# Optimization experiments

Hardware: AMD Instinct MI355X
Metric: run time of the kernel (lower is better)

The kernel has to match this reference:

```python
import jax, jax.numpy as jnp
import numpy as np

N = 32768      # total nodes
B = 64         # graphs
NPG = 512      # nodes per graph
E = 524288     # edges (avg degree 16)
H = 4          # heads
Fh = 64        # per-head dim
C = H * Fh     # 256
FIN = 128
RATIO = 0.5


def gat(x, src, dst, W, a_src, a_dst, bias, n_nodes):
    # PyG GATConv: linear -> add self-loops -> edge softmax over dst -> scatter-add
    h = (x @ W).reshape(n_nodes, H, Fh)
    loop = jnp.arange(n_nodes)
    s = jnp.concatenate([src, loop])
    d = jnp.concatenate([dst, loop])
    es = jnp.sum(h * a_src, axis=-1)  # [N,H]
    ed = jnp.sum(h * a_dst, axis=-1)  # [N,H]
    e = jax.nn.leaky_relu(es[s] + ed[d], 0.2)  # [E+N,H]
    m = jax.ops.segment_max(e, d, num_segments=n_nodes)
    ex = jnp.exp(e - m[d])
    den = jax.ops.segment_sum(ex, d, num_segments=n_nodes)
    alpha = ex / (den[d] + 1e-16)  # [E+N,H]
    out = jax.ops.segment_sum(alpha[:, :, None] * h[s], d, num_segments=n_nodes)
    return out.reshape(n_nodes, C) + bias


def pool(x, sw, sb, tw, tb, n_graphs, n_per):
    # equal-size graphs -> per-graph top-k as a batched top_k
    k = max(1, int(n_per * RATIO))
    scores = jax.nn.sigmoid(x @ sw + sb)[:, 0].reshape(n_graphs, n_per)
    _, idx = jax.lax.top_k(scores, k)  # [B,k]
    xb = x.reshape(n_graphs, n_per, x.shape[-1])
    sel = jnp.take_along_axis(xb, idx[:, :, None], axis=1)
    sel = sel.reshape(n_graphs * k, x.shape[-1])
    return sel @ tw + tb, k


def setup_inputs() -> dict:
    key = jax.random.key(0)
    ks = jax.random.split(key, 24)
    x = jax.random.normal(ks[0], (N, FIN), dtype=jnp.float32)
    # within-graph random edges
    gbase = jnp.repeat(jnp.arange(B, dtype=jnp.int32) * NPG, E // B)
    src = gbase + jax.random.randint(ks[1], (E,), 0, NPG)
    dst = gbase + jax.random.randint(ks[2], (E,), 0, NPG)
    edge_index = jnp.stack([src, dst]).astype(jnp.int32)
    batch = jnp.repeat(jnp.arange(B, dtype=jnp.int32), NPG)
    def lin(k, fi, fo):
        return jax.random.normal(k, (fi, fo), dtype=jnp.float32) / np.sqrt(fi)
    inp = dict(x=x, edge_index=edge_index, batch=batch)
    inp["W1"] = lin(ks[3], FIN, C)
    inp["a_src1"] = jax.random.normal(ks[4], (H, Fh), jnp.float32) / np.sqrt(Fh)
    inp["a_dst1"] = jax.random.normal(ks[5], (H, Fh), jnp.float32) / np.sqrt(Fh)
    inp["b1"] = jnp.zeros((C,), jnp.float32)
    inp["W2"] = lin(ks[6], C, C)
    inp["a_src2"] = jax.random.normal(ks[7], (H, Fh), jnp.float32) / np.sqrt(Fh)
    inp["a_dst2"] = jax.random.normal(ks[8], (H, Fh), jnp.float32) / np.sqrt(Fh)
    inp["b2"] = jnp.zeros((C,), jnp.float32)
    inp["p1_sw"] = lin(ks[9], C, 1)
    inp["p1_sb"] = jnp.zeros((1,), jnp.float32)
    inp["p1_tw"] = lin(ks[10], C, C)
    inp["p1_tb"] = jnp.zeros((C,), jnp.float32)
    inp["p2_sw"] = lin(ks[11], C, 1)
    inp["p2_sb"] = jnp.zeros((1,), jnp.float32)
    inp["p2_tw"] = lin(ks[12], C, C)
    inp["p2_tb"] = jnp.zeros((C,), jnp.float32)
    inp["c1w"] = lin(ks[13], C, 64)
    inp["c1b"] = jnp.zeros((64,), jnp.float32)
    inp["c2w"] = lin(ks[14], 64, 2)
    inp["c2b"] = jnp.zeros((2,), jnp.float32)
    return inp


def reference(x, edge_index, batch, W1, a_src1, a_dst1, b1, W2, a_src2, a_dst2, b2,
              p1_sw, p1_sb, p1_tw, p1_tb, p2_sw, p2_sb, p2_tw, p2_tb,
              c1w, c1b, c2w, c2b):
    src, dst = edge_index[0], edge_index[1]
    h = jax.nn.elu(gat(x, src, dst, W1, a_src1, a_dst1, b1, N))
    h = jax.nn.elu(gat(h, src, dst, W2, a_src2, a_dst2, b2, N))
    # pool1 then pool2 (edge_index after pooling is never consumed by the output path)
    h, k1 = pool(h, p1_sw, p1_sb, p1_tw, p1_tb, B, NPG)
    h, k2 = pool(h, p2_sw, p2_sb, p2_tw, p2_tb, B, k1)
    g = h.reshape(B, k2, C).mean(axis=1)  # global mean pool per graph
    g = jax.nn.relu(g @ c1w + c1b)
    g = g @ c2w + c2b
    return jax.nn.log_softmax(g, axis=1)
```

## Files before the change

kernel.cpp:

```cpp
#include <hip/hip_runtime.h>
#include <hip/hip_bf16.h>
#include <hip/hip_fp16.h>
#include <math.h>

constexpr int NN  = 32768;
constexpr int BG  = 64;
constexpr int NPG = 512;
constexpr int EG  = 524288;
constexpr int EPG = EG / BG;
constexpr int HH  = 4;
constexpr int FH  = 64;
constexpr int CC  = 256;
constexpr int FIN = 128;
constexpr int KP1 = 256;
constexpr int KP2 = 128;
constexpr int NS  = 4;

typedef __attribute__((ext_vector_type(8))) short short8;
typedef __attribute__((ext_vector_type(4))) float f32x4;

__device__ inline float leaky02(float v) { return v > 0.0f ? v : 0.2f * v; }

__device__ inline unsigned short f2bf(float v) {
    __hip_bfloat16 h = __float2bfloat16(v);
    return *(unsigned short*)&h;
}
__device__ inline float bf2f(unsigned short u) {
    __hip_bfloat16 h;
    *(unsigned short*)&h = u;
    return __bfloat162float(h);
}
__device__ inline void split2(float v, unsigned short& hi, unsigned short& lo) {
    hi = f2bf(v);
    lo = f2bf(v - bf2f(hi));
}
__device__ inline void split8(const float* p, short8& hi, short8& lo) {
    const float4 f0 = *(const float4*)p;
    const float4 f1 = *(const float4*)(p + 4);
    unsigned short h, l;
    split2(f0.x, h, l); hi[0] = (short)h; lo[0] = (short)l;
    split2(f0.y, h, l); hi[1] = (short)h; lo[1] = (short)l;
    split2(f0.z, h, l); hi[2] = (short)h; lo[2] = (short)l;
    split2(f0.w, h, l); hi[3] = (short)h; lo[3] = (short)l;
    split2(f1.x, h, l); hi[4] = (short)h; lo[4] = (short)l;
    split2(f1.y, h, l); hi[5] = (short)h; lo[5] = (short)l;
    split2(f1.z, h, l); hi[6] = (short)h; lo[6] = (short)l;
    split2(f1.w, h, l); hi[7] = (short)h; lo[7] = (short)l;
}

__device__ inline unsigned short f2h(float v) {
    __half h = __float2half(v);
    return *(unsigned short*)&h;
}

__device__ inline unsigned int fmap(float v) {
    unsigned int b = __float_as_uint(v);
    return (b & 0x80000000u) ? ~b : (b | 0x80000000u);
}

__device__ inline void acc8h(const unsigned short* p, float a, float* acc) {
    const uint4 u = *(const uint4*)p;
    const __half2* hp = (const __half2*)&u;
    const float2 f0 = __half22float2(hp[0]);
    const float2 f1 = __half22float2(hp[1]);
    const float2 f2 = __half22float2(hp[2]);
    const float2 f3 = __half22float2(hp[3]);
    acc[0] = fmaf(a, f0.x, acc[0]); acc[1] = fmaf(a, f0.y, acc[1]);
    acc[2] = fmaf(a, f1.x, acc[2]); acc[3] = fmaf(a, f1.y, acc[3]);
    acc[4] = fmaf(a, f2.x, acc[4]); acc[5] = fmaf(a, f2.y, acc[5]);
    acc[6] = fmaf(a, f3.x, acc[6]); acc[7] = fmaf(a, f3.y, acc[7]);
}

__global__ __launch_bounds__(1024) void setup_k(
        const int* __restrict__ src, const int* __restrict__ dst,
        int* __restrict__ rowp, int* __restrict__ esrc,
        const float* __restrict__ tw1, const float* __restrict__ sw2,
        const float* __restrict__ tb1, const float* __restrict__ sb2,
        float* __restrict__ w12, float* __restrict__ b12,
        const float* __restrict__ tw2, const float* __restrict__ c1w,
        const float* __restrict__ tb2, float* __restrict__ T,
        float* __restrict__ bc2,
        const float* __restrict__ W1, const float* __restrict__ W2,
        unsigned short* __restrict__ w1ph, unsigned short* __restrict__ w1pl,
        unsigned short* __restrict__ w2ph, unsigned short* __restrict__ w2pl) {
    __shared__ int lcnt[NPG];
    __shared__ int lofs[NPG];
    const int b = blockIdx.x;
    const int t = threadIdx.x;
    if (b < BG) {
        const int g = b;
        const int ebase = g * EPG;
        const int nbase = g * NPG;
        if (t < NPG) lcnt[t] = 0;
        __syncthreads();
        int ds[EPG / 1024];
#pragma unroll
        for (int j = 0; j < EPG / 1024; ++j) {
            ds[j] = dst[ebase + t + 1024 * j] - nbase;
            atomicAdd(&lcnt[ds[j]], 1);
        }
        __syncthreads();
        if (t < NPG) lofs[t] = lcnt[t];
        __syncthreads();
        for (int o = 1; o < NPG; o <<= 1) {
            int v = 0;
            if (t < NPG && t >= o) v = lofs[t - o];
            __syncthreads();
            if (t < NPG) lofs[t] += v;
            __syncthreads();
        }
        if (t < NPG) {
            int ex = lofs[t] - lcnt[t];
            rowp[nbase + t] = ebase + ex;
            lcnt[t] = ex;
        }
        if (g == BG - 1 && t == 0) rowp[NN] = EG;
        __syncthreads();
#pragma unroll
        for (int j = 0; j < EPG / 1024; ++j) {
            int p = atomicAdd(&lcnt[ds[j]], 1);
            esrc[ebase + p] = src[ebase + t + 1024 * j];
        }
        return;
    }
    if (t >= 256) return;
    const int pb = b - BG;
    if (pb < 66) {
        if (pb == 0) {
            float s = 0.0f;
            for (int o = 0; o < CC; ++o) s += tw1[t * CC + o] * sw2[o];
            w12[t] = s;
            if (t == 0) {
                float bb = 0.0f;
                for (int o = 0; o < CC; ++o) bb += tb1[o] * sw2[o];
                *b12 = bb + sb2[0];
            }
        } else if (pb < 65) {
            const int r = (pb - 1) * 4 + (t >> 6);
            const int cth = t & 63;
            float s = 0.0f;
            for (int j = 0; j < CC; ++j) s = fmaf(tw2[r * CC + j], c1w[j * 64 + cth], s);
            T[r * 64 + cth] = s;
        } else if (t < 64) {
            float s = 0.0f;
            for (int j = 0; j < CC; ++j) s = fmaf(tb2[j], c1w[j * 64 + t], s);
            bc2[t] = s;
        }
    } else {
        const int idx = (pb - 66) * 256 + t;
        if (idx < 4096) {
            const int nt = idx >> 8, rem = idx & 255;
            const int kg = rem >> 6, l = rem & 63;
            const int n = nt * 16 + (l & 15);
            const int kb = kg * 32 + (l >> 4) * 8;
            unsigned short h[8], lo[8];
#pragma unroll
            for (int j = 0; j < 8; ++j) split2(W1[(kb + j) * CC + n], h[j], lo[j]);
#pragma unroll
            for (int j = 0; j < 8; ++j) {
                w1ph[(size_t)idx * 8 + j] = h[j];
                w1pl[(size_t)idx * 8 + j] = lo[j];
            }
        } else {
            const int i2 = idx - 4096;
            const int nt = i2 >> 9, rem = i2 & 511;
            const int kg = rem >> 6, l = rem & 63;
            const int n = nt * 16 + (l & 15);
            const int kb = kg * 32 + (l >> 4) * 8;
            unsigned short h[8], lo[8];
#pragma unroll
            for (int j = 0; j < 8; ++j) split2(W2[(kb + j) * CC + n], h[j], lo[j]);
#pragma unroll
            for (int j = 0; j < 8; ++j) {
                w2ph[(size_t)i2 * 8 + j] = h[j];
                w2pl[(size_t)i2 * 8 + j] = lo[j];
            }
        }
    }
}

__global__ __launch_bounds__(256, 4) void gemm_mfma_attn(
        const unsigned short* __restrict__ Ahi, const unsigned short* __restrict__ Alo,
        const unsigned short* __restrict__ Bph, const unsigned short* __restrict__ Bpl,
        unsigned short* __restrict__ Cb, int K,
        const float* __restrict__ a_src, const float* __restrict__ a_dst,
        float* __restrict__ es, float* __restrict__ ed) {
    const int t = threadIdx.x;
    const int w = t >> 6;
    const int l = t & 63;
    const int bx   = blockIdx.x;
    const int xcd  = bx & 7;
    const int slot = bx >> 3;
    const int gph  = xcd + ((slot >> 4) << 3);
    const int row0 = gph * NPG + ((slot & 15) << 5);
    const int m = l & 15;
    const int q = l >> 4;
    const int ncol0 = w * 64;
    const int KG = K >> 5;

    const unsigned short* aH0 = Ahi + (size_t)(row0 + m) * K + q * 8;
    const unsigned short* aL0 = Alo + (size_t)(row0 + m) * K + q * 8;
    const unsigned short* aH1 = aH0 + (size_t)16 * K;
    const unsigned short* aL1 = aL0 + (size_t)16 * K;

    f32x4 acc0[4], acc1[4];
#pragma unroll
    for (int c = 0; c < 4; ++c) {
        acc0[c] = (f32x4){0.f, 0.f, 0.f, 0.f};
        acc1[c] = (f32x4){0.f, 0.f, 0.f, 0.f};
    }

    for (int kg = 0; kg < KG; ++kg) {
        const int ko = kg * 32;
        short8 ah0 = *(const short8*)(aH0 + ko);
        short8 al0 = *(const short8*)(aL0 + ko);
        short8 ah1 = *(const short8*)(aH1 + ko);
        short8 al1 = *(const short8*)(aL1 + ko);
#pragma unroll
        for (int c = 0; c < 4; ++c) {
            const int nt = (w << 2) + c;
            const size_t boff = ((size_t)(nt * KG + kg) * 64 + l) * 8;
            short8 bh = *(const short8*)(Bph + boff);
            short8 bl = *(const short8*)(Bpl + boff);
            acc0[c] = __builtin_amdgcn_mfma_f32_16x16x32_bf16(ah0, bh, acc0[c], 0, 0, 0);
            acc0[c] = __builtin_amdgcn_mfma_f32_16x16x32_bf16(ah0, bl, acc0[c], 0, 0, 0);
            acc0[c] = __builtin_amdgcn_mfma_f32_16x16x32_bf16(al0, bh, acc0[c], 0, 0, 0);
            acc1[c] = __builtin_amdgcn_mfma_f32_16x16x32_bf16(ah1, bh, acc1[c], 0, 0, 0);
            acc1[c] = __builtin_amdgcn_mfma_f32_16x16x32_bf16(ah1, bl, acc1[c], 0, 0, 0);
            acc1[c] = __builtin_amdgcn_mfma_f32_16x16x32_bf16(al1, bh, acc1[c], 0, 0, 0);
        }
    }

#pragma unroll
    for (int c = 0; c < 4; ++c)
#pragma unroll
        for (int r = 0; r < 4; ++r) {
            Cb[(size_t)(row0 + q * 4 + r) * CC + ncol0 + c * 16 + m] = f2h(acc0[c][r]);
            Cb[(size_t)(row0 + 16 + q * 4 + r) * CC + ncol0 + c * 16 + m] = f2h(acc1[c][r]);
        }

    float asv[4], adv[4];
#pragma unroll
    for (int c = 0; c < 4; ++c) {
        asv[c] = a_src[ncol0 + c * 16 + m];
        adv[c] = a_dst[ncol0 + c * 16 + m];
    }
#pragma unroll
    for (int r = 0; r < 4; ++r) {
        float ps0 = 0.f, pd0 = 0.f, ps1 = 0.f, pd1 = 0.f;
#pragma unroll
        for (int c = 0; c < 4; ++c) {
            ps0 = fmaf(acc0[c][r], asv[c], ps0);
            pd0 = fmaf(acc0[c][r], adv[c], pd0);
            ps1 = fmaf(acc1[c][r], asv[c], ps1);
            pd1 = fmaf(acc1[c][r], adv[c], pd1);
        }
#pragma unroll
        for (int o = 8; o >= 1; o >>= 1) {
            ps0 += __shfl_down(ps0, o, 16);
            pd0 += __shfl_down(pd0, o, 16);
            ps1 += __shfl_down(ps1, o, 16);
            pd1 += __shfl_down(pd1, o, 16);
        }
        if (m == 0) {
            es[(row0 + q * 4 + r) * HH + w] = ps0;
            ed[(row0 + q * 4 + r) * HH + w] = pd0;
            es[(row0 + 16 + q * 4 + r) * HH + w] = ps1;
            ed[(row0 + 16 + q * 4 + r) * HH + w] = pd1;
        }
    }
}

__global__ __launch_bounds__(256, 4) void gemm_mfma_attn_f32(
        const float* __restrict__ Af,
        const unsigned short* __restrict__ Bph, const unsigned short* __restrict__ Bpl,
        unsigned short* __restrict__ Cb, int K,
        const float* __restrict__ a_src, const float* __restrict__ a_dst,
        float* __restrict__ es, float* __restrict__ ed,
        const float* __restrict__ tw1, const float* __restrict__ T,
        const float* __restrict__ tb1, const float* __restrict__ bc2,
        const float* __restrict__ c1b, float* __restrict__ Wc,
        float* __restrict__ bcv) {
    const int t = threadIdx.x;
    const int bx = blockIdx.x;
    if (bx >= NN / 32) {
        const int fb = bx - NN / 32;
        if (fb < 64) {
            const int r = fb * 4 + (t >> 6);
            const int cth = t & 63;
            float s = 0.0f;
            for (int j = 0; j < CC; ++j) s = fmaf(tw1[r * CC + j], T[j * 64 + cth], s);
            Wc[r * 64 + cth] = s;
        } else if (t < 64) {
            float s = 0.0f;
            for (int j = 0; j < CC; ++j) s = fmaf(tb1[j], T[j * 64 + t], s);
            bcv[t] = s + bc2[t] + c1b[t];
        }
        return;
    }
    const int w = t >> 6;
    const int l = t & 63;
    const int xcd  = bx & 7;
    const int slot = bx >> 3;
    const int gph  = xcd + ((slot >> 4) << 3);
    const int row0 = gph * NPG + ((slot & 15) << 5);
    const int m = l & 15;
    const int q = l >> 4;
    const int ncol0 = w * 64;
    const int KG = K >> 5;

    const float* aF0 = Af + (size_t)(row0 + m) * K + q * 8;
    const float* aF1 = aF0 + (size_t)16 * K;

    f32x4 acc0[4], acc1[4];
#pragma unroll
    for (int c = 0; c < 4; ++c) {
        acc0[c] = (f32x4){0.f, 0.f, 0.f, 0.f};
        acc1[c] = (f32x4){0.f, 0.f, 0.f, 0.f};
    }

    for (int kg = 0; kg < KG; ++kg) {
        const int ko = kg * 32;
        short8 ah0, al0, ah1, al1;
        split8(aF0 + ko, ah0, al0);
        split8(aF1 + ko, ah1, al1);
#pragma unroll
        for (int c = 0; c < 4; ++c) {
            const int nt = (w << 2) + c;
            const size_t boff = ((size_t)(nt * KG + kg) * 64 + l) * 8;
            short8 bh = *(const short8*)(Bph + boff);
            short8 bl = *(const short8*)(Bpl + boff);
            acc0[c] = __builtin_amdgcn_mfma_f32_16x16x32_bf16(ah0, bh, acc0[c], 0, 0, 0);
            acc0[c] = __builtin_amdgcn_mfma_f32_16x16x32_bf16(ah0, bl, acc0[c], 0, 0, 0);
            acc0[c] = __builtin_amdgcn_mfma_f32_16x16x32_bf16(al0, bh, acc0[c], 0, 0, 0);
            acc1[c] = __builtin_amdgcn_mfma_f32_16x16x32_bf16(ah1, bh, acc1[c], 0, 0, 0);
            acc1[c] = __builtin_amdgcn_mfma_f32_16x16x32_bf16(ah1, bl, acc1[c], 0, 0, 0);
            acc1[c] = __builtin_amdgcn_mfma_f32_16x16x32_bf16(al1, bh, acc1[c], 0, 0, 0);
        }
    }

#pragma unroll
    for (int c = 0; c < 4; ++c)
#pragma unroll
        for (int r = 0; r < 4; ++r) {
            Cb[(size_t)(row0 + q * 4 + r) * CC + ncol0 + c * 16 + m] = f2h(acc0[c][r]);
            Cb[(size_t)(row0 + 16 + q * 4 + r) * CC + ncol0 + c * 16 + m] = f2h(acc1[c][r]);
        }

    float asv[4], adv[4];
#pragma unroll
    for (int c = 0; c < 4; ++c) {
        asv[c] = a_src[ncol0 + c * 16 + m];
        adv[c] = a_dst[ncol0 + c * 16 + m];
    }
#pragma unroll
    for (int r = 0; r < 4; ++r) {
        float ps0 = 0.f, pd0 = 0.f, ps1 = 0.f, pd1 = 0.f;
#pragma unroll
        for (int c = 0; c < 4; ++c) {
            ps0 = fmaf(acc0[c][r], asv[c], ps0);
            pd0 = fmaf(acc0[c][r], adv[c], pd0);
            ps1 = fmaf(acc1[c][r], asv[c], ps1);
            pd1 = fmaf(acc1[c][r], adv[c], pd1);
        }
#pragma unroll
        for (int o = 8; o >= 1; o >>= 1) {
            ps0 += __shfl_down(ps0, o, 16);
            pd0 += __shfl_down(pd0, o, 16);
            ps1 += __shfl_down(ps1, o, 16);
            pd1 += __shfl_down(pd1, o, 16);
        }
        if (m == 0) {
            es[(row0 + q * 4 + r) * HH + w] = ps0;
            ed[(row0 + q * 4 + r) * HH + w] = pd0;
            es[(row0 + 16 + q * 4 + r) * HH + w] = ps1;
            ed[(row0 + 16 + q * 4 + r) * HH + w] = pd1;
        }
    }
}

__global__ __launch_bounds__(256) void gat_edge(const unsigned short* __restrict__ zh,
                                                const int* __restrict__ rowp,
                                                const int* __restrict__ esrc,
                                                const float* __restrict__ es,
                                                const float* __restrict__ ed,
                                                const float* __restrict__ bias,
                                                float* __restrict__ out,
                                                unsigned short* __restrict__ outh,
                                                unsigned short* __restrict__ outl,
                                                const float* __restrict__ sw1,
                                                const float* __restrict__ sb1,
                                                const float* __restrict__ w12,
                                                const float* __restrict__ b12,
                                                float* __restrict__ sc1,
                                                float* __restrict__ sc2) {
    const int w = threadIdx.x >> 6;
    const int l = threadIdx.x & 63;
    const int b    = blockIdx.x;
    const int xcd  = b & 7;
    const int slot = b >> 3;
    const int gph  = xcd + ((slot >> 7) << 3);
    const int d    = gph * NPG + ((slot & 127) << 2) + w;

    const int h    = l & 3;
    const int ei   = l >> 2;
    const int lh   = l & 31;
    const int half = l >> 5;
    const int hcol = lh >> 3;
    const int c0   = lh << 3;

    const int beg = rowp[d];
    const int deg = rowp[d + 1] - beg;

    float acc[8];
#pragma unroll
    for (int i = 0; i < 8; ++i) acc[i] = 0.0f;

    if (deg <= 16 * NS) {
        const float edh = ed[d * HH + h];
        int   sidx[NS];
        float v[NS];
#pragma unroll
        for (int j = 0; j < NS; ++j) { sidx[j] = d; v[j] = 0.0f; }
        float vmax = -INFINITY, eself = 0.0f, vself = 0.0f;
        if (ei == 0) {
            vself = leaky02(es[d * HH + h] + edh);
            vmax = vself;
        }
#pragma unroll
        for (int j = 0; j < NS; ++j) {
            int i = ei + 16 * j;
            if (i < deg) {
                sidx[j] = esrc[beg + i];
                v[j] = leaky02(es[sidx[j] * HH + h] + edh);
                vmax = fmaxf(vmax, v[j]);
            }
        }
#pragma unroll
        for (int o = 4; o <= 32; o <<= 1) vmax = fmaxf(vmax, __shfl_xor(vmax, o));
        float dsum = 0.0f;
#pragma unroll
        for (int j = 0; j < NS; ++j) {
            int i = ei + 16 * j;
            if (i < deg) { v[j] = __expf(v[j] - vmax); dsum += v[j]; }
        }
        if (ei == 0) { eself = __expf(vself - vmax); dsum += eself; }
#pragma unroll
        for (int o = 4; o <= 32; o <<= 1) dsum += __shfl_xor(dsum, o);
        const float inv = 1.0f / (dsum + 1e-16f);
#pragma unroll
        for (int j = 0; j < NS; ++j) v[j] *= inv;
        eself *= inv;

        float aself = __shfl(eself, hcol);
        if (half) aself = 0.0f;
        acc8h(zh + (size_t)d * CC + c0, aself, acc);

#pragma unroll
        for (int j = 0; j < NS; ++j) {
            if (16 * j < deg) {
#pragma unroll
                for (int rr = 0; rr < 8; ++rr) {
                    if (16 * j + 2 * rr < deg) {
                        const int slb  = (2 * rr + half) << 2;
                        const int srcn = __shfl(sidx[j], slb);
                        const float a  = __shfl(v[j], slb + hcol);
                        acc8h(zh + (size_t)srcn * CC + c0, a, acc);
                    }
                }
            }
        }
    } else {
        const float edh = ed[d * HH + h];
        float vmax = (ei == 0) ? leaky02(es[d * HH + h] + edh) : -INFINITY;
        for (int i = ei; i < deg; i += 16)
            vmax = fmaxf(vmax, leaky02(es[esrc[beg + i] * HH + h] + edh));
#pragma unroll
        for (int o = 4; o <= 32; o <<= 1) vmax = fmaxf(vmax, __shfl_xor(vmax, o));
        float dsum = (ei == 0) ? __expf(leaky02(es[d * HH + h] + edh) - vmax) : 0.0f;
        for (int i = ei; i < deg; i += 16)
            dsum += __expf(leaky02(es[esrc[beg + i] * HH + h] + edh) - vmax);
#pragma unroll
        for (int o = 4; o <= 32; o <<= 1) dsum += __shfl_xor(dsum, o);
        const float inv = 1.0f / (dsum + 1e-16f);

        const float vmaxc = __shfl(vmax, hcol);
        const float invc  = __shfl(inv,  hcol);
        const float edh4  = ed[d * HH + hcol];
        float a0 = __expf(leaky02(es[d * HH + hcol] + edh4) - vmaxc) * invc;
        if (half) a0 = 0.0f;
        acc8h(zh + (size_t)d * CC + c0, a0, acc);
        for (int e = half; e < deg; e += 2) {
            const int srcn = esrc[beg + e];
            const float a = __expf(leaky02(es[srcn * HH + hcol] + edh4) - vmaxc) * invc;
            acc8h(zh + (size_t)srcn * CC + c0, a, acc);
        }
    }

#pragma unroll
    for (int i = 0; i < 8; ++i) acc[i] += __shfl_xor(acc[i], 32);

    const int cw = c0 + (half << 2);
    float o0 = half ? acc[4] : acc[0];
    float o1 = half ? acc[5] : acc[1];
    float o2 = half ? acc[6] : acc[2];
    float o3 = half ? acc[7] : acc[3];

    const float4 bv = *(const float4*)(bias + cw);
    o0 += bv.x; o0 = o0 > 0.0f ? o0 : expm1f(o0);
    o1 += bv.y; o1 = o1 > 0.0f ? o1 : expm1f(o1);
    o2 += bv.z; o2 = o2 > 0.0f ? o2 : expm1f(o2);
    o3 += bv.w; o3 = o3 > 0.0f ? o3 : expm1f(o3);

    if (out) *(float4*)(out + (size_t)d * CC + cw) = make_float4(o0, o1, o2, o3);
    if (outh) {
        ushort4 uh, ul;
        split2(o0, uh.x, ul.x);
        split2(o1, uh.y, ul.y);
        split2(o2, uh.z, ul.z);
        split2(o3, uh.w, ul.w);
        *(ushort4*)(outh + (size_t)d * CC + cw) = uh;
        *(ushort4*)(outl + (size_t)d * CC + cw) = ul;
    }

    if (sc1) {
        const float4 s1 = *(const float4*)(sw1 + cw);
        const float4 s2 = *(const float4*)(w12 + cw);
        float r1 = o0 * s1.x + o1 * s1.y + o2 * s1.z + o3 * s1.w;
        float r2 = o0 * s2.x + o1 * s2.y + o2 * s2.z + o3 * s2.w;
#pragma unroll
        for (int off = 32; off >= 1; off >>= 1) {
            r1 += __shfl_xor(r1, off);
            r2 += __shfl_xor(r2, off);
        }
        if (l == 0) {
            sc1[d] = r1 + sb1[0];
            sc2[d] = r2 + b12[0];
        }
    }
}

__global__ __launch_bounds__(512) void pool_g(const float* __restrict__ sc1,
                                              const float* __restrict__ sc2,
                                              const float* __restrict__ feat,
                                              const float* __restrict__ Wc,
                                              const float* __restrict__ bc,
                                              const float* __restrict__ c2w,
                                              const float* __restrict__ c2b,
                                              float* __restrict__ outp) {
    __shared__ int wcnt[2][8];
    __shared__ int ecnt[8];
    __shared__ int ccnt[8];
    __shared__ int list[KP2];
    __shared__ float v0[CC];
    __shared__ float vbuf[2][CC];
    __shared__ float part[4][64];
    __shared__ float v2[64];
    const int g = blockIdx.x;
    const int t = threadIdx.x;
    const int lane = t & 63, wid = t >> 6;
    const unsigned long long lmask = (1ull << lane) - 1ull;

    const unsigned int u1 = fmap(sc1[(size_t)g * NPG + t]);
    unsigned int p = 0;
    int pp = 0;
    for (int bb = 31; bb >= 0; --bb) {
        const unsigned int cand = p | (1u << bb);
        unsigned long long bal = __ballot(u1 >= cand);
        if (lane == 0) wcnt[pp][wid] = __popcll(bal);
        __syncthreads();
        int c = 0;
#pragma unroll
        for (int i = 0; i < 8; ++i) c += wcnt[pp][i];
        if (c >= KP1) p = cand;
        pp ^= 1;
    }
    int cgt;
    {
        unsigned long long bal = __ballot(u1 > p);
        if (lane == 0) wcnt[pp][wid] = __popcll(bal);
        __syncthreads();
        cgt = 0;
#pragma unroll
        for (int i = 0; i < 8; ++i) cgt += wcnt[pp][i];
        pp ^= 1;
    }
    int keep1;
    {
        const int eq = (u1 == p);
        unsigned long long bal = __ballot(eq);
        if (lane == 0) ecnt[wid] = __popcll(bal);
        __syncthreads();
        int pre = 0;
        for (int i = 0; i < wid; ++i) pre += ecnt[i];
        const int eqrank = pre + __popcll(bal & lmask);
        keep1 = (u1 > p) || (eq && eqrank < (KP1 - cgt));
    }
    __syncthreads();

    const unsigned int u2 = keep1 ? fmap(sc2[(size_t)g * NPG + t]) : 0u;
    p = 0;
    for (int bb = 31; bb >= 0; --bb) {
        const unsigned int cand = p | (1u << bb);
        unsigned long long bal = __ballot(u2 >= cand);
        if (lane == 0) wcnt[pp][wid] = __popcll(bal);
        __syncthreads();
        int c = 0;
#pragma unroll
        for (int i = 0; i < 8; ++i) c += wcnt[pp][i];
        if (c >= KP2) p = cand;
        pp ^= 1;
    }
    {
        unsigned long long bal = __ballot(u2 > p);
        if (lane == 0) wcnt[pp][wid] = __popcll(bal);
        __syncthreads();
        cgt = 0;
#pragma unroll
        for (int i = 0; i < 8; ++i) cgt += wcnt[pp][i];
        pp ^= 1;
    }
    int keep2;
    {
        const int eq = (u2 == p);
        unsigned long long bal = __ballot(eq);
        if (lane == 0) ccnt[wid] = __popcll(bal);
        __syncthreads();
        int pre = 0;
        for (int i = 0; i < wid; ++i) pre += ccnt[i];
        const int eqrank = pre + __popcll(bal & lmask);
        keep2 = (u2 > p) || (eq && eqrank < (KP2 - cgt));
    }
    __syncthreads();

    {
        unsigned long long bal = __ballot(keep2);
        if (lane == 0) ecnt[wid] = __popcll(bal);
        __syncthreads();
        int pre = 0;
        for (int i = 0; i < wid; ++i) pre += ecnt[i];
        const int pos = pre + __popcll(bal & lmask);
        if (keep2) list[pos] = t;
    }
    __syncthreads();

    {
        const int col = t & (CC - 1);
        const int hf = t >> 8;
        float acc = 0.0f;
        for (int i = hf * 64; i < hf * 64 + 64; ++i)
            acc += feat[((size_t)g * NPG + list[i]) * CC + col];
        vbuf[hf][col] = acc;
    }
    __syncthreads();
    if (t < CC) v0[t] = (vbuf[0][t] + vbuf[1][t]) * (1.0f / KP2);
    __syncthreads();

    if (t < 256) {
        const int q = t >> 6, cth = t & 63;
        float pr = 0.0f;
        for (int j = q * 64; j < q * 64 + 64; ++j)
            pr = fmaf(v0[j], Wc[j * 64 + cth], pr);
        part[q][cth] = pr;
    }
    __syncthreads();
    if (t < 64) {
        float u = bc[t];
#pragma unroll
        for (int q = 0; q < 4; ++q) u += part[q][t];
        v2[t] = fmaxf(u, 0.0f);
    }
    __syncthreads();
    if (t < 2) {
        float o = c2b[t];
        for (int j = 0; j < 64; ++j) o = fmaf(v2[j], c2w[j * 2 + t], o);
        part[0][t] = o;
    }
    __syncthreads();
    if (t == 0) {
        float a = part[0][0], bq = part[0][1];
        float mx = fmaxf(a, bq);
        float lse = mx + logf(expf(a - mx) + expf(bq - mx));
        outp[g * 2 + 0] = a - lse;
        outp[g * 2 + 1] = bq - lse;
    }
}

extern "C" void kernel_launch(void* const* d_in, const int* in_sizes, int n_in,
                              void* d_out, int out_size, void* d_ws, size_t ws_size,
                              hipStream_t stream) {
    const float* x      = (const float*)d_in[0];
    const int*   ei     = (const int*)d_in[1];
    const int*   src    = ei;
    const int*   dst    = ei + EG;
    const float* W1     = (const float*)d_in[3];
    const float* a_src1 = (const float*)d_in[4];
    const float* a_dst1 = (const float*)d_in[5];
    const float* b1     = (const float*)d_in[6];
    const float* W2     = (const float*)d_in[7];
    const float* a_src2 = (const float*)d_in[8];
    const float* a_dst2 = (const float*)d_in[9];
    const float* b2     = (const float*)d_in[10];
    const float* p1_sw  = (const float*)d_in[11];
    const float* p1_sb  = (const float*)d_in[12];
    const float* p1_tw  = (const float*)d_in[13];
    const float* p1_tb  = (const float*)d_in[14];
    const float* p2_sw  = (const float*)d_in[15];
    const float* p2_sb  = (const float*)d_in[16];
    const float* p2_tw  = (const float*)d_in[17];
    const float* p2_tb  = (const float*)d_in[18];
    const float* c1w    = (const float*)d_in[19];
    const float* c1b    = (const float*)d_in[20];
    const float* c2w    = (const float*)d_in[21];
    const float* c2b    = (const float*)d_in[22];
    float* out = (float*)d_out;

    float* ws = (float*)d_ws;
    float* z = ws;
    unsigned short* zh = (unsigned short*)z;
    float* fregion = z + (size_t)NN * CC;
    unsigned short* fhi = (unsigned short*)fregion;
    unsigned short* flo = fhi + (size_t)NN * CC;
    float* featF = fregion;
    float* wsp = fregion + (size_t)NN * CC;
    unsigned short* w1ph = (unsigned short*)wsp;
    unsigned short* w1pl = w1ph + 256 * FIN;
    unsigned short* w2ph = w1pl + 256 * FIN;
    unsigned short* w2pl = w2ph + 256 * CC;
    float* es  = (float*)(w2pl + 256 * CC);
    float* ed  = es + NN * HH;
    int* rowp  = (int*)(ed + NN * HH);
    int* esrc  = rowp + NN + 1;
    float* sc1 = (float*)(esrc + EG);
    float* sc2 = sc1 + NN;
    int* sel1  = (int*)(sc2 + NN);
    float* w12 = (float*)(sel1 + NN);
    float* b12 = w12 + CC;
    float* T   = b12 + 64;
    float* Wc  = T + CC * 64;
    float* bc2 = Wc + CC * 64;
    float* bcv = bc2 + 64;

    setup_k<<<BG + 66 + 48, 1024, 0, stream>>>(
        src, dst, rowp, esrc,
        p1_tw, p2_sw, p1_tb, p2_sb, w12, b12, p2_tw, c1w, p2_tb, T, bc2,
        W1, W2, w1ph, w1pl, w2ph, w2pl);

    gemm_mfma_attn_f32<<<NN / 32 + 65, 256, 0, stream>>>(
        x, w1ph, w1pl, zh, FIN, a_src1, a_dst1, es, ed,
        p1_tw, T, p1_tb, bc2, c1b, Wc, bcv);
    gat_edge<<<NN / 4, 256, 0, stream>>>(zh, rowp, esrc, es, ed, b1,
                                         nullptr, fhi, flo,
                                         nullptr, nullptr, nullptr, nullptr,
                                         nullptr, nullptr);

    gemm_mfma_attn<<<NN / 32, 256, 0, stream>>>(fhi, flo, w2ph, w2pl, zh, CC,
                                                a_src2, a_dst2, es, ed);
    gat_edge<<<NN / 4, 256, 0, stream>>>(zh, rowp, esrc, es, ed, b2,
                                         featF, nullptr, nullptr,
                                         p1_sw, p1_sb, w12, b12, sc1, sc2);

    pool_g<<<BG, 512, 0, stream>>>(sc1, sc2, featF, Wc, bcv, c2w, c2b, out);
}
```

Before: 265.7 us.

## Use packed FMA accumulators, wave-shuffle prefix scan, and fast ELU exp

Switches the GAT aggregation accumulators to 2-wide float vectors so the compiler can emit packed FMA instructions. Replaces the shared-memory Hillis-Steele scan in the CSR setup with a two-level wavefront shuffle scan, which needs fewer barriers. Replaces expm1f in the ELU with __expf minus one, which is cheaper but less accurate for small negative inputs.

After: 261.0 us. No clear change (-1.8%).

```diff
diff --git a/kernel.cpp b/kernel.cpp
--- a/kernel.cpp
+++ b/kernel.cpp
@@ -18,6 +18,7 @@
 
 typedef __attribute__((ext_vector_type(8))) short short8;
 typedef __attribute__((ext_vector_type(4))) float f32x4;
+typedef __attribute__((ext_vector_type(2))) float f32x2v;
 
 __device__ inline float leaky02(float v) { return v > 0.0f ? v : 0.2f * v; }
 
@@ -58,17 +59,16 @@
     return (b & 0x80000000u) ? ~b : (b | 0x80000000u);
 }
 
-__device__ inline void acc8h(const unsigned short* p, float a, float* acc) {
+__device__ inline void acc8h(const unsigned short* p, float a, f32x2v* acc) {
     const uint4 u = *(const uint4*)p;
     const __half2* hp = (const __half2*)&u;
-    const float2 f0 = __half22float2(hp[0]);
-    const float2 f1 = __half22float2(hp[1]);
-    const float2 f2 = __half22float2(hp[2]);
-    const float2 f3 = __half22float2(hp[3]);
-    acc[0] = fmaf(a, f0.x, acc[0]); acc[1] = fmaf(a, f0.y, acc[1]);
-    acc[2] = fmaf(a, f1.x, acc[2]); acc[3] = fmaf(a, f1.y, acc[3]);
-    acc[4] = fmaf(a, f2.x, acc[4]); acc[5] = fmaf(a, f2.y, acc[5]);
-    acc[6] = fmaf(a, f3.x, acc[6]); acc[7] = fmaf(a, f3.y, acc[7]);
+    f32x2v av; av[0] = a; av[1] = a;
+#pragma unroll
+    for (int i = 0; i < 4; ++i) {
+        const float2 f = __half22float2(hp[i]);
+        f32x2v fv; fv[0] = f.x; fv[1] = f.y;
+        acc[i] = __builtin_elementwise_fma(fv, av, acc[i]);
+    }
 }
 
 __global__ __launch_bounds__(1024) void setup_k(
@@ -84,7 +84,7 @@
         unsigned short* __restrict__ w1ph, unsigned short* __restrict__ w1pl,
         unsigned short* __restrict__ w2ph, unsigned short* __restrict__ w2pl) {
     __shared__ int lcnt[NPG];
-    __shared__ int lofs[NPG];
+    __shared__ int wsum[8];
     const int b = blockIdx.x;
     const int t = threadIdx.x;
     if (b < BG) {
@@ -100,17 +100,31 @@
             atomicAdd(&lcnt[ds[j]], 1);
         }
         __syncthreads();
-        if (t < NPG) lofs[t] = lcnt[t];
-        __syncthreads();
-        for (int o = 1; o < NPG; o <<= 1) {
-            int v = 0;
-            if (t < NPG && t >= o) v = lofs[t - o];
-            __syncthreads();
-            if (t < NPG) lofs[t] += v;
-            __syncthreads();
-        }
+        int c = 0, sInc = 0;
         if (t < NPG) {
-            int ex = lofs[t] - lcnt[t];
+            c = lcnt[t];
+            sInc = c;
+#pragma unroll
+            for (int o = 1; o < 64; o <<= 1) {
+                int v = __shfl_up(sInc, o);
+                if ((t & 63) >= o) sInc += v;
+            }
+            if ((t & 63) == 63) wsum[t >> 6] = sInc;
+        }
+        __syncthreads();
+        if (t < 8) {
+            int v = wsum[t];
+            int s = v;
+#pragma unroll
+            for (int o = 1; o < 8; o <<= 1) {
+                int u2 = __shfl_up(s, o, 8);
+                if (t >= o) s += u2;
+            }
+            wsum[t] = s - v;
+        }
+        __syncthreads();
+        if (t < NPG) {
+            const int ex = sInc - c + wsum[t >> 6];
             rowp[nbase + t] = ebase + ex;
             lcnt[t] = ex;
         }
@@ -412,9 +426,9 @@
     const int beg = rowp[d];
     const int deg = rowp[d + 1] - beg;
 
-    float acc[8];
-#pragma unroll
-    for (int i = 0; i < 8; ++i) acc[i] = 0.0f;
+    f32x2v acc[4];
+#pragma unroll
+    for (int i = 0; i < 4; ++i) acc[i] = (f32x2v){0.f, 0.f};
 
     if (deg <= 16 * NS) {
         const float edh = ed[d * HH + h];
@@ -498,19 +512,23 @@
     }
 
 #pragma unroll
-    for (int i = 0; i < 8; ++i) acc[i] += __shfl_xor(acc[i], 32);
+    for (int i = 0; i < 4; ++i) {
+        float a0 = acc[i][0]; a0 += __shfl_xor(a0, 32);
+        float a1 = acc[i][1]; a1 += __shfl_xor(a1, 32);
+        acc[i][0] = a0; acc[i][1] = a1;
+    }
 
     const int cw = c0 + (half << 2);
-    float o0 = half ? acc[4] : acc[0];
-    float o1 = half ? acc[5] : acc[1];
-    float o2 = half ? acc[6] : acc[2];
-    float o3 = half ? acc[7] : acc[3];
+    float o0 = half ? acc[2][0] : acc[0][0];
+    float o1 = half ? acc[2][1] : acc[0][1];
+    float o2 = half ? acc[3][0] : acc[1][0];
+    float o3 = half ? acc[3][1] : acc[1][1];
 
     const float4 bv = *(const float4*)(bias + cw);
-    o0 += bv.x; o0 = o0 > 0.0f ? o0 : expm1f(o0);
-    o1 += bv.y; o1 = o1 > 0.0f ? o1 : expm1f(o1);
-    o2 += bv.z; o2 = o2 > 0.0f ? o2 : expm1f(o2);
-    o3 += bv.w; o3 = o3 > 0.0f ? o3 : expm1f(o3);
+    o0 += bv.x; o0 = o0 > 0.0f ? o0 : __expf(o0) - 1.0f;
+    o1 += bv.y; o1 = o1 > 0.0f ? o1 : __expf(o1) - 1.0f;
+    o2 += bv.z; o2 = o2 > 0.0f ? o2 : __expf(o2) - 1.0f;
+    o3 += bv.w; o3 = o3 > 0.0f ? o3 : __expf(o3) - 1.0f;
 
     if (out) *(float4*)(out + (size_t)d * CC + cw) = make_float4(o0, o1, o2, o3);
     if (outh) {
```
